# Kernel tuning notes

Measured on AMD Instinct MI355X. Metric: run time of the kernel, lower is better.

Reference implementation:

```python
import jax, jax.numpy as jnp
import numpy as np

N, DIN, D, HID, E, OUT = 16384, 1024, 1024, 256, 10, 1024


def setup_inputs() -> dict:
    key = jax.random.key(0)
    ks = jax.random.split(key, 13)
    g = lambda k, sh, s=0.02: (jax.random.normal(k, sh, jnp.float32) * s)
    return {
        "x": jax.random.normal(ks[0], (N, DIN), jnp.float32),
        "top_k": 2,
        # input projection (input_dim -> adjusted_dim)
        "Wp": g(ks[1], (DIN, D)), "bp": jnp.zeros((D,), jnp.float32),
        # MHA with seq_len=1 reduces exactly to out_proj(v_proj(x))
        "Wv": g(ks[2], (D, D)), "bv": jnp.zeros((D,), jnp.float32),
        "Wo": g(ks[3], (D, D)), "bo": jnp.zeros((D,), jnp.float32),
        # gate
        "Wg": g(ks[4], (D, E)), "bg": jnp.zeros((E,), jnp.float32),
        # experts: Linear(D,256) -> ReLU -> Linear(256,OUT), stacked over E
        "W1": g(ks[5], (E, D, HID)), "b1": jnp.zeros((E, HID), jnp.float32),
        "W2": g(ks[6], (E, HID, OUT)), "b2": jnp.zeros((E, OUT), jnp.float32),
    }


def reference(x, top_k, Wp, bp, Wv, bv, Wo, bo, Wg, bg, W1, b1, W2, b2):
    n = x.shape[0]
    e = Wg.shape[1]
    h = x @ Wp + bp                               # [N, D] input projection
    # MultiheadAttention with seq_len=1: softmax over one key == 1 exactly,
    # so attn output == out_proj(v_proj(h)).
    a = (h @ Wv + bv) @ Wo + bo                   # [N, D]
    gate_probs = jax.nn.softmax(a @ Wg + bg, axis=-1)   # [N, E]
    vals, idx = jax.lax.top_k(gate_probs, top_k)        # [N, K]
    vals = vals / jnp.sum(vals, axis=-1, keepdims=True)
    # scatter normalized top-k probs into dense combine weights [N, E]
    combine = jnp.zeros((n, e), a.dtype).at[jnp.arange(n)[:, None], idx].set(vals)
    # dense all-expert MLP, masked by combine weights (zeros kill unrouted experts)
    hid = jax.nn.relu(jnp.einsum("nd,edh->enh", a, W1) + b1[:, None, :])  # [E, N, HID]
    hid = hid * combine.T[:, :, None]                                      # weight tokens
    out = jnp.einsum("enh,eho->no", hid, W2) + combine @ b2                # [N, OUT]
    return out
```

## Files before the change

kernel.cpp:

```cpp
#include <hip/hip_runtime.h>
#include <hip/hip_bf16.h>
#include <math.h>

#define N_TOK   16384
#define D_IN    1024
#define D_MODEL 1024
#define HID     256
#define NEXP    10
#define D_OUT   1024

#define EPAD 128
#define A_CAP (2*N_TOK + NEXP*EPAD)

typedef __attribute__((ext_vector_type(8))) __bf16 bf16x8;
typedef __attribute__((ext_vector_type(4))) float floatx4;

__device__ __forceinline__ int xcd_chunk(int orig, int nwg)
{
    const int q = nwg >> 3, r = nwg & 7;
    const int c = orig & 7, j = orig >> 3;
    return (c < r ? c * (q + 1) : r * (q + 1) + (c - r) * q) + j;
}

__device__ __forceinline__ bf16x8 lds_frag(const short* base, int row, int chunk)
{
    return *(const bf16x8*)(base + row * 64 + (chunk << 3));
}

__device__ __forceinline__ void tile_plain(const short* As, const short* Bs,
                                           int wm, int wn, int lane, floatx4 acc[4][4])
{
    const int m15 = lane & 15, quad = lane >> 4, sw = m15 & 7;
#pragma unroll
    for (int kk = 0; kk < 2; ++kk) {
        bf16x8 af[4], bfr[4];
#pragma unroll
        for (int i = 0; i < 4; ++i)
            af[i] = lds_frag(As, wm * 64 + i * 16 + m15, ((kk << 2) + quad) ^ sw);
#pragma unroll
        for (int j = 0; j < 4; ++j)
            bfr[j] = lds_frag(Bs, wn * 64 + j * 16 + m15, ((kk << 2) + quad) ^ sw);
#pragma unroll
        for (int i = 0; i < 4; ++i)
#pragma unroll
            for (int j = 0; j < 4; ++j)
                acc[i][j] = __builtin_amdgcn_mfma_f32_16x16x32_bf16(af[i], bfr[j],
                                                                    acc[i][j], 0, 0, 0);
    }
}

__device__ __forceinline__ void tile_split(const short* As, const short* Bs,
                                           int wm, int wn, int lane, floatx4 acc[4][4])
{
    const int m15 = lane & 15, quad = lane >> 4, sw = m15 & 7;
    bf16x8 ah[4], al[4], bh[4], bl[4];
#pragma unroll
    for (int i = 0; i < 4; ++i) {
        int r = wm * 64 + i * 16 + m15;
        ah[i] = lds_frag(As, r, quad ^ sw);
        al[i] = lds_frag(As, r, (4 + quad) ^ sw);
    }
#pragma unroll
    for (int j = 0; j < 4; ++j) {
        int r = wn * 64 + j * 16 + m15;
        bh[j] = lds_frag(Bs, r, quad ^ sw);
        bl[j] = lds_frag(Bs, r, (4 + quad) ^ sw);
    }
#pragma unroll
    for (int i = 0; i < 4; ++i)
#pragma unroll
        for (int j = 0; j < 4; ++j) {
            floatx4 c = acc[i][j];
            c = __builtin_amdgcn_mfma_f32_16x16x32_bf16(ah[i], bh[j], c, 0, 0, 0);
            c = __builtin_amdgcn_mfma_f32_16x16x32_bf16(ah[i], bl[j], c, 0, 0, 0);
            c = __builtin_amdgcn_mfma_f32_16x16x32_bf16(al[i], bh[j], c, 0, 0, 0);
            acc[i][j] = c;
        }
}

__global__ __launch_bounds__(256)
void gemm_split_kernel(const __hip_bfloat16* Ahi_, const __hip_bfloat16* Alo_,
                       const __hip_bfloat16* Bhi_, const __hip_bfloat16* Blo_,
                       const float* __restrict__ bias,
                       __hip_bfloat16* Chi_, __hip_bfloat16* Clo_, int K, int N)
{
    __shared__ __align__(16) short As[128 * 64];
    __shared__ __align__(16) short Bs[128 * 64];
    const short* Ahi = (const short*)Ahi_;
    const short* Alo = (const short*)Alo_;
    const short* Bhi = (const short*)Bhi_;
    const short* Blo = (const short*)Blo_;

    const int tid = threadIdx.x, lane = tid & 63, w = tid >> 6;
    const int wm = w & 1, wn = w >> 1;
    const int lin = blockIdx.y * gridDim.x + blockIdx.x;
    const int lgc = xcd_chunk(lin, gridDim.x * gridDim.y);
    const int row0 = (lgc / gridDim.x) * 128, col0 = (lgc % gridDim.x) * 128;
    const int lr = lane >> 3;
    const int g = (lane & 7) ^ lr;
    const int plane = g >> 2, colel = (g & 3) * 8;

    const short* pA[4];
    const short* pB[4];
#pragma unroll
    for (int i = 0; i < 4; ++i) {
        int r = w * 32 + i * 8 + lr;
        pA[i] = (plane ? Alo : Ahi) + (size_t)(row0 + r) * K + colel;
        pB[i] = (plane ? Blo : Bhi) + (size_t)(col0 + r) * K + colel;
    }

    floatx4 acc[4][4];
#pragma unroll
    for (int i = 0; i < 4; ++i)
#pragma unroll
        for (int j = 0; j < 4; ++j) acc[i][j] = (floatx4)(0.f);

    bf16x8 va[4], vb[4];
#pragma unroll
    for (int i = 0; i < 4; ++i) {
        va[i] = *(const bf16x8*)(pA[i]);
        vb[i] = *(const bf16x8*)(pB[i]);
    }

    for (int k0 = 0; k0 < K; k0 += 32) {
        __syncthreads();
#pragma unroll
        for (int i = 0; i < 4; ++i) {
            *(bf16x8*)(&As[(w * 32 + i * 8) * 64 + lane * 8]) = va[i];
            *(bf16x8*)(&Bs[(w * 32 + i * 8) * 64 + lane * 8]) = vb[i];
        }
        __syncthreads();
        if (k0 + 32 < K) {
#pragma unroll
            for (int i = 0; i < 4; ++i) {
                va[i] = *(const bf16x8*)(pA[i] + k0 + 32);
                vb[i] = *(const bf16x8*)(pB[i] + k0 + 32);
            }
        }
        tile_split(As, Bs, wm, wn, lane, acc);
    }

    const int m15 = lane & 15, quad = lane >> 4;
#pragma unroll
    for (int i = 0; i < 4; ++i) {
#pragma unroll
        for (int t = 0; t < 4; ++t) {
            int row = row0 + wm * 64 + i * 16 + quad * 4 + t;
            size_t rb = (size_t)row * N;
#pragma unroll
            for (int j = 0; j < 4; ++j) {
                int col = col0 + wn * 64 + j * 16 + m15;
                float v = acc[i][j][t] + bias[col];
                __hip_bfloat16 hi = __float2bfloat16(v);
                Chi_[rb + col] = hi;
                if (Clo_) Clo_[rb + col] = __float2bfloat16(v - __bfloat162float(hi));
            }
        }
    }
}

__global__ __launch_bounds__(256)
void expert1_kernel(const __hip_bfloat16* a_, const __hip_bfloat16* W1t_,
                    const float* __restrict__ b1,
                    const int* __restrict__ assign_token, const int* __restrict__ offs,
                    const __hip_bfloat16* zrow_, __hip_bfloat16* hid_)
{
    __shared__ __align__(16) short As[128 * 64];
    __shared__ __align__(16) short Bs[128 * 64];
    const short* A = (const short*)a_;
    const short* zrow = (const short*)zrow_;

    const int tid = threadIdx.x, lane = tid & 63, w = tid >> 6;
    const int wm = w & 1, wn = w >> 1;
    const int lin = blockIdx.y * gridDim.x + blockIdx.x;
    const int lgc = xcd_chunk(lin, gridDim.x * gridDim.y);
    const int row0 = (lgc / gridDim.x) * 128, col0 = (lgc % gridDim.x) * 128;
    const int lr = lane >> 3, g = (lane & 7) ^ lr, colel = g * 8;

    int e = NEXP - 1;
    for (int q = 0; q < NEXP; ++q) { if (row0 < offs[q + 1]) { e = q; break; } }
    const short* B = (const short*)W1t_ + (size_t)e * HID * D_MODEL;

    const short* pA[4];
    const short* pB[4];
#pragma unroll
    for (int i = 0; i < 4; ++i) {
        int r = w * 32 + i * 8 + lr;
        int tok = assign_token[row0 + r];
        pA[i] = (tok >= 0 ? A + (size_t)tok * D_MODEL : zrow) + colel;
        pB[i] = B + (size_t)(col0 + r) * D_MODEL + colel;
    }

    floatx4 acc[4][4];
#pragma unroll
    for (int i = 0; i < 4; ++i)
#pragma unroll
        for (int j = 0; j < 4; ++j) acc[i][j] = (floatx4)(0.f);

    bf16x8 va[4], vb[4];
#pragma unroll
    for (int i = 0; i < 4; ++i) {
        va[i] = *(const bf16x8*)(pA[i]);
        vb[i] = *(const bf16x8*)(pB[i]);
    }

    for (int k0 = 0; k0 < D_MODEL; k0 += 64) {
        __syncthreads();
#pragma unroll
        for (int i = 0; i < 4; ++i) {
            *(bf16x8*)(&As[(w * 32 + i * 8) * 64 + lane * 8]) = va[i];
            *(bf16x8*)(&Bs[(w * 32 + i * 8) * 64 + lane * 8]) = vb[i];
        }
        __syncthreads();
        if (k0 + 64 < D_MODEL) {
#pragma unroll
            for (int i = 0; i < 4; ++i) {
                va[i] = *(const bf16x8*)(pA[i] + k0 + 64);
                vb[i] = *(const bf16x8*)(pB[i] + k0 + 64);
            }
        }
        tile_plain(As, Bs, wm, wn, lane, acc);
    }

    const int m15 = lane & 15, quad = lane >> 4;
#pragma unroll
    for (int i = 0; i < 4; ++i) {
#pragma unroll
        for (int t = 0; t < 4; ++t) {
            int row = row0 + wm * 64 + i * 16 + quad * 4 + t;
            size_t rb = (size_t)row * HID;
#pragma unroll
            for (int j = 0; j < 4; ++j) {
                int col = col0 + wn * 64 + j * 16 + m15;
                float v = acc[i][j][t] + b1[(size_t)e * HID + col];
                hid_[rb + col] = __float2bfloat16(fmaxf(v, 0.f));
            }
        }
    }
}

__global__ __launch_bounds__(256)
void expert2_kernel(const __hip_bfloat16* hid_, const __hip_bfloat16* W2t_,
                    const int* __restrict__ offs, __hip_bfloat16* exp_out_)
{
    __shared__ __align__(16) short As[128 * 64];
    __shared__ __align__(16) short Bs[128 * 64];
    const short* A = (const short*)hid_;

    const int tid = threadIdx.x, lane = tid & 63, w = tid >> 6;
    const int wm = w & 1, wn = w >> 1;
    const int lin = blockIdx.y * gridDim.x + blockIdx.x;
    const int lgc = xcd_chunk(lin, gridDim.x * gridDim.y);
    const int row0 = (lgc / gridDim.x) * 128, col0 = (lgc % gridDim.x) * 128;
    const int lr = lane >> 3, g = (lane & 7) ^ lr, colel = g * 8;

    int e = NEXP - 1;
    for (int q = 0; q < NEXP; ++q) { if (row0 < offs[q + 1]) { e = q; break; } }
    const short* B = (const short*)W2t_ + (size_t)e * D_OUT * HID;

    const short* pA[4];
    const short* pB[4];
#pragma unroll
    for (int i = 0; i < 4; ++i) {
        int r = w * 32 + i * 8 + lr;
        pA[i] = A + (size_t)(row0 + r) * HID + colel;
        pB[i] = B + (size_t)(col0 + r) * HID + colel;
    }

    floatx4 acc[4][4];
#pragma unroll
    for (int i = 0; i < 4; ++i)
#pragma unroll
        for (int j = 0; j < 4; ++j) acc[i][j] = (floatx4)(0.f);

    bf16x8 va[4], vb[4];
#pragma unroll
    for (int i = 0; i < 4; ++i) {
        va[i] = *(const bf16x8*)(pA[i]);
        vb[i] = *(const bf16x8*)(pB[i]);
    }

    for (int k0 = 0; k0 < HID; k0 += 64) {
        __syncthreads();
#pragma unroll
        for (int i = 0; i < 4; ++i) {
            *(bf16x8*)(&As[(w * 32 + i * 8) * 64 + lane * 8]) = va[i];
            *(bf16x8*)(&Bs[(w * 32 + i * 8) * 64 + lane * 8]) = vb[i];
        }
        __syncthreads();
        if (k0 + 64 < HID) {
#pragma unroll
            for (int i = 0; i < 4; ++i) {
                va[i] = *(const bf16x8*)(pA[i] + k0 + 64);
                vb[i] = *(const bf16x8*)(pB[i] + k0 + 64);
            }
        }
        tile_plain(As, Bs, wm, wn, lane, acc);
    }

    const int m15 = lane & 15, quad = lane >> 4;
#pragma unroll
    for (int i = 0; i < 4; ++i) {
#pragma unroll
        for (int t = 0; t < 4; ++t) {
            int row = row0 + wm * 64 + i * 16 + quad * 4 + t;
            size_t rb = (size_t)row * D_OUT;
#pragma unroll
            for (int j = 0; j < 4; ++j) {
                int col = col0 + wn * 64 + j * 16 + m15;
                exp_out_[rb + col] = __float2bfloat16(acc[i][j][t]);
            }
        }
    }
}

__global__ __launch_bounds__(256)
void convert_gate_kernel(const float* __restrict__ x, const float* __restrict__ MgT,
                         const float* __restrict__ bgeff,
                         __hip_bfloat16* __restrict__ x_hi, __hip_bfloat16* __restrict__ x_lo,
                         int* __restrict__ route_e, float* __restrict__ route_w)
{
    const int wave = threadIdx.x >> 6, lane = threadIdx.x & 63;
    const int n = blockIdx.x * 4 + wave;
    const float* xrow = x + (size_t)n * D_IN;

    float4 v[4];
#pragma unroll
    for (int it = 0; it < 4; ++it)
        v[it] = *(const float4*)(xrow + it * 256 + lane * 4);

    float p[NEXP];
#pragma unroll
    for (int e = 0; e < NEXP; ++e) p[e] = 0.f;

#pragma unroll
    for (int it = 0; it < 4; ++it) {
        const int d = it * 256 + lane * 4;
        union { __hip_bfloat16 b[4]; short4 s; } uh, ul;
        uh.b[0] = __float2bfloat16(v[it].x); ul.b[0] = __float2bfloat16(v[it].x - __bfloat162float(uh.b[0]));
        uh.b[1] = __float2bfloat16(v[it].y); ul.b[1] = __float2bfloat16(v[it].y - __bfloat162float(uh.b[1]));
        uh.b[2] = __float2bfloat16(v[it].z); ul.b[2] = __float2bfloat16(v[it].z - __bfloat162float(uh.b[2]));
        uh.b[3] = __float2bfloat16(v[it].w); ul.b[3] = __float2bfloat16(v[it].w - __bfloat162float(uh.b[3]));
        *(short4*)(x_hi + (size_t)n * D_IN + d) = uh.s;
        *(short4*)(x_lo + (size_t)n * D_IN + d) = ul.s;
#pragma unroll
        for (int e = 0; e < NEXP; ++e) {
            const float4 m = *(const float4*)(MgT + (size_t)e * 1024 + d);
            p[e] += v[it].x * m.x + v[it].y * m.y + v[it].z * m.z + v[it].w * m.w;
        }
    }

#pragma unroll
    for (int e = 0; e < NEXP; ++e) {
        float t = p[e];
        for (int off = 32; off > 0; off >>= 1) t += __shfl_down(t, off);
        p[e] = t;
    }
    if (lane == 0) {
        float lg[NEXP];
#pragma unroll
        for (int e = 0; e < NEXP; ++e) lg[e] = p[e] + bgeff[e];
        int e0 = 0; float v0 = lg[0];
        for (int e = 1; e < NEXP; ++e) if (lg[e] > v0) { v0 = lg[e]; e0 = e; }
        int e1 = -1; float v1 = -3.0e38f;
        for (int e = 0; e < NEXP; ++e) {
            if (e == e0) continue;
            if (lg[e] > v1) { v1 = lg[e]; e1 = e; }
        }
        float w0 = 1.f / (1.f + expf(v1 - v0));
        float w1 = 1.f - w0;
        route_e[n * 2]     = e0;
        route_e[n * 2 + 1] = e1;
        route_w[n * 2]     = w0;
        route_w[n * 2 + 1] = w1;
    }
}

__global__ __launch_bounds__(256)
void count_kernel(const int* __restrict__ route_e, int* __restrict__ counts)
{
    __shared__ int h[NEXP];
    if (threadIdx.x < NEXP) h[threadIdx.x] = 0;
    __syncthreads();
    const int i = blockIdx.x * 512 + threadIdx.x;
    atomicAdd(&h[route_e[i]], 1);
    atomicAdd(&h[route_e[i + 256]], 1);
    __syncthreads();
    if (threadIdx.x < NEXP) atomicAdd(&counts[threadIdx.x], h[threadIdx.x]);
}

__global__ __launch_bounds__(256)
void transpose_cvt_kernel(const float* __restrict__ in, __hip_bfloat16* out_hi,
                          __hip_bfloat16* out_lo, int R, int C)
{
    __shared__ float t[32][33];
    const size_t zoff = (size_t)blockIdx.z * R * C;
    in += zoff; out_hi += zoff; if (out_lo) out_lo += zoff;
    const int c0 = blockIdx.x * 32, r0 = blockIdx.y * 32;
    const int tx = threadIdx.x & 31, ty = threadIdx.x >> 5;
#pragma unroll
    for (int i = 0; i < 4; ++i)
        t[ty + i * 8][tx] = in[(size_t)(r0 + ty + i * 8) * C + (c0 + tx)];
    __syncthreads();
#pragma unroll
    for (int i = 0; i < 4; ++i) {
        float v = t[tx][ty + i * 8];
        size_t o = (size_t)(c0 + ty + i * 8) * R + (r0 + tx);
        __hip_bfloat16 hi = __float2bfloat16(v);
        out_hi[o] = hi;
        if (out_lo) out_lo[o] = __float2bfloat16(v - __bfloat162float(hi));
    }
}

__global__ __launch_bounds__(256)
void convert_plain_kernel(const float* __restrict__ in,
                          __hip_bfloat16* __restrict__ out_hi,
                          __hip_bfloat16* __restrict__ out_lo)
{
    const int i = blockIdx.x * 256 + threadIdx.x;
    const float4 v = ((const float4*)in)[i];
    union { __hip_bfloat16 b[4]; short4 s; } uh, ul;
    uh.b[0] = __float2bfloat16(v.x); ul.b[0] = __float2bfloat16(v.x - __bfloat162float(uh.b[0]));
    uh.b[1] = __float2bfloat16(v.y); ul.b[1] = __float2bfloat16(v.y - __bfloat162float(uh.b[1]));
    uh.b[2] = __float2bfloat16(v.z); ul.b[2] = __float2bfloat16(v.z - __bfloat162float(uh.b[2]));
    uh.b[3] = __float2bfloat16(v.w); ul.b[3] = __float2bfloat16(v.w - __bfloat162float(uh.b[3]));
    ((short4*)out_hi)[i] = uh.s;
    ((short4*)out_lo)[i] = ul.s;
}

__global__ __launch_bounds__(256)
void bias2_kernel(const float* __restrict__ bp, const float* __restrict__ bv,
                  const float* __restrict__ bo,
                  const __hip_bfloat16* __restrict__ Pt_hi,
                  const __hip_bfloat16* __restrict__ Pt_lo,
                  const __hip_bfloat16* __restrict__ Wot_hi,
                  const __hip_bfloat16* __restrict__ Wot_lo,
                  float* __restrict__ beff2)
{
    const int wave = threadIdx.x >> 6, lane = threadIdx.x & 63;
    const int n = blockIdx.x * 4 + wave;
    float acc = 0.f;
    for (int k = lane; k < D_MODEL; k += 64) {
        const size_t o = (size_t)n * D_MODEL + k;
        float pt = __bfloat162float(Pt_hi[o]) + __bfloat162float(Pt_lo[o]);
        float wo = __bfloat162float(Wot_hi[o]) + __bfloat162float(Wot_lo[o]);
        acc += bp[k] * pt + bv[k] * wo;
    }
    for (int off = 32; off > 0; off >>= 1) acc += __shfl_down(acc, off);
    if (lane == 0) beff2[n] = acc + bo[n];
}

__global__ __launch_bounds__(256)
void wchain_kernel(const float* __restrict__ A, const float* __restrict__ B,
                   float* __restrict__ Cm, int trans)
{
    const int wave = threadIdx.x >> 6, lane = threadIdx.x & 63;
    const int m = blockIdx.x * 4 + wave;
    float acc[NEXP];
#pragma unroll
    for (int e = 0; e < NEXP; ++e) acc[e] = 0.f;
    const float* ar = A + (size_t)m * 1024;
    for (int d = lane; d < 1024; d += 64) {
        float av = ar[d];
        const float* br = B + (size_t)d * NEXP;
#pragma unroll
        for (int e = 0; e < NEXP; ++e) acc[e] += av * br[e];
    }
#pragma unroll
    for (int e = 0; e < NEXP; ++e) {
        float v = acc[e];
        for (int off = 32; off > 0; off >>= 1) v += __shfl_down(v, off);
        if (lane == 0) Cm[trans ? ((size_t)e * 1024 + m) : ((size_t)m * NEXP + e)] = v;
    }
}

__global__ __launch_bounds__(256)
void bias_eff_kernel(const float* __restrict__ bp, const float* __restrict__ bv,
                     const float* __restrict__ bo, const float* __restrict__ bg,
                     const float* __restrict__ Wg, const float* __restrict__ t1,
                     const float* __restrict__ t2, float* __restrict__ bgeff)
{
    __shared__ float red[256];
    const int tid = threadIdx.x;
    float acc[NEXP];
#pragma unroll
    for (int e = 0; e < NEXP; ++e) acc[e] = 0.f;
    for (int d = tid; d < 1024; d += 256) {
        float o = bo[d], v = bv[d], p = bp[d];
#pragma unroll
        for (int e = 0; e < NEXP; ++e)
            acc[e] += o * Wg[d * NEXP + e] + v * t1[d * NEXP + e] + p * t2[d * NEXP + e];
    }
    for (int e = 0; e < NEXP; ++e) {
        red[tid] = acc[e];
        __syncthreads();
        for (int s = 128; s > 0; s >>= 1) {
            if (tid < s) red[tid] += red[tid + s];
            __syncthreads();
        }
        if (tid == 0) bgeff[e] = red[0] + bg[e];
        __syncthreads();
    }
}

__global__ __launch_bounds__(256)
void init_kernel(int* __restrict__ counts, int* __restrict__ cursors,
                 int* __restrict__ assign_token, int* __restrict__ zrow_i,
                 float* __restrict__ fzero)
{
    int i = blockIdx.x * 256 + threadIdx.x;
    if (i < NEXP) { counts[i] = 0; cursors[i] = 0; }
    if (i < 512) zrow_i[i] = 0;
    if (i < 1024) fzero[i] = 0.f;
    if (i < A_CAP) assign_token[i] = -1;
}

__global__ void offsets_kernel(const int* __restrict__ counts, int* __restrict__ offs)
{
    if (threadIdx.x == 0 && blockIdx.x == 0) {
        int acc = 0;
        for (int e = 0; e < NEXP; ++e) {
            offs[e] = acc;
            acc += (counts[e] + EPAD - 1) / EPAD * EPAD;
        }
        offs[NEXP] = acc;
    }
}

__global__ __launch_bounds__(256)
void scatter_kernel(const int* __restrict__ route_e,
                    const int* __restrict__ offs, int* __restrict__ cursors,
                    int* __restrict__ assign_token, int* __restrict__ slot_of)
{
    const int i = blockIdx.x * 256 + threadIdx.x;
    const int lane = threadIdx.x & 63;
    const int e = route_e[i];
    int slot = 0;
#pragma unroll
    for (int q = 0; q < NEXP; ++q) {
        unsigned long long mask = __ballot(e == q);
        if (e == q) {
            const int leader = (int)__ffsll((long long)mask) - 1;
            const int rank = (int)__popcll(mask & ((1ull << lane) - 1ull));
            int base = 0;
            if (lane == leader) base = atomicAdd(&cursors[q], (int)__popcll(mask));
            base = __shfl(base, leader);
            slot = offs[q] + base + rank;
        }
    }
    assign_token[slot] = i >> 1;
    slot_of[i] = slot;
}

__global__ __launch_bounds__(256)
void combine_kernel(const __hip_bfloat16* __restrict__ exp_out,
                    const int* __restrict__ slot_of, const int* __restrict__ route_e,
                    const float* __restrict__ route_w, const float* __restrict__ b2,
                    float* __restrict__ out)
{
    const int n = blockIdx.x;
    const int c = threadIdx.x * 4;
    const int s0 = slot_of[n * 2],  s1 = slot_of[n * 2 + 1];
    const int e0 = route_e[n * 2],  e1 = route_e[n * 2 + 1];
    const float w0 = route_w[n * 2], w1 = route_w[n * 2 + 1];

    union U { float2 f2; __hip_bfloat16 b[4]; } u0, u1;
    u0.f2 = *(const float2*)(exp_out + (size_t)s0 * D_OUT + c);
    u1.f2 = *(const float2*)(exp_out + (size_t)s1 * D_OUT + c);
    const float4 bb0 = *(const float4*)(b2 + (size_t)e0 * D_OUT + c);
    const float4 bb1 = *(const float4*)(b2 + (size_t)e1 * D_OUT + c);

    float4 o;
    o.x = w0 * (__bfloat162float(u0.b[0]) + bb0.x) + w1 * (__bfloat162float(u1.b[0]) + bb1.x);
    o.y = w0 * (__bfloat162float(u0.b[1]) + bb0.y) + w1 * (__bfloat162float(u1.b[1]) + bb1.y);
    o.z = w0 * (__bfloat162float(u0.b[2]) + bb0.z) + w1 * (__bfloat162float(u1.b[2]) + bb1.z);
    o.w = w0 * (__bfloat162float(u0.b[3]) + bb0.w) + w1 * (__bfloat162float(u1.b[3]) + bb1.w);
    *(float4*)(out + (size_t)n * D_OUT + c) = o;
}

extern "C" void kernel_launch(void* const* d_in, const int* in_sizes, int n_in,
                              void* d_out, int out_size, void* d_ws, size_t ws_size,
                              hipStream_t stream)
{
    const float* x  = (const float*)d_in[0];
    const float* Wp = (const float*)d_in[2];
    const float* bp = (const float*)d_in[3];
    const float* Wv = (const float*)d_in[4];
    const float* bv = (const float*)d_in[5];
    const float* Wo = (const float*)d_in[6];
    const float* bo = (const float*)d_in[7];
    const float* Wg = (const float*)d_in[8];
    const float* bg = (const float*)d_in[9];
    const float* W1 = (const float*)d_in[10];
    const float* b1 = (const float*)d_in[11];
    const float* W2 = (const float*)d_in[12];
    const float* b2 = (const float*)d_in[13];
    float* out = (float*)d_out;

    char* W = (char*)d_ws;
    typedef __hip_bfloat16 bf;
    bf* x_hi  = (bf*)(W + 0);
    bf* x_lo  = (bf*)(W + 33554432);
    bf* a_bf  = (bf*)(W + 100663296);
    bf* exp_out = (bf*)(W + 0);
    bf* hid   = (bf*)(W + 69730304);
    bf* Wvr_hi = (bf*)(W + 88080384);
    bf* Wvr_lo = (bf*)(W + 90177536);
    bf* Wpr_hi = (bf*)(W + 92274688);
    bf* Wpr_lo = (bf*)(W + 94371840);
    float* fzero = (float*)(W + 96468992);
    float* beff2 = (float*)(W + 96473088);
    bf* Pt_hi  = (bf*)(W + 134217728);
    bf* Pt_lo  = (bf*)(W + 136314880);
    bf* Mt_hi  = (bf*)(W + 138412032);
    bf* Mt_lo  = (bf*)(W + 140509184);
    bf* Wot_hi = (bf*)(W + 142606336);
    bf* Wot_lo = (bf*)(W + 144703488);
    bf* W1t    = (bf*)(W + 146800640);
    bf* W2t    = (bf*)(W + 152043520);
    bf*    zrow         = (bf*)(W + 157286400);
    int*   route_e      = (int*)(W + 157288448);
    float* route_w      = (float*)(W + 157419520);
    int*   slot_of      = (int*)(W + 157550592);
    int*   assign_token = (int*)(W + 157681664);
    int*   counts       = (int*)(W + 157817856);
    int*   offs         = (int*)(W + 157817920);
    int*   cursors      = (int*)(W + 157817984);
    float* MgT          = (float*)(W + 157818048);
    float* t1           = (float*)(W + 157859008);
    float* t2           = (float*)(W + 157899968);
    float* bgeff        = (float*)(W + 157940928);

    dim3 blk(256);

    init_kernel<<<(A_CAP + 255) / 256, blk, 0, stream>>>(counts, cursors, assign_token,
                                                         (int*)zrow, fzero);

    transpose_cvt_kernel<<<dim3(32, 32, 1), blk, 0, stream>>>(Wo, Wot_hi, Wot_lo, D_MODEL, D_MODEL);
    convert_plain_kernel<<<1024, blk, 0, stream>>>(Wv, Wvr_hi, Wvr_lo);
    convert_plain_kernel<<<1024, blk, 0, stream>>>(Wp, Wpr_hi, Wpr_lo);
    transpose_cvt_kernel<<<dim3(HID / 32, D_MODEL / 32, NEXP), blk, 0, stream>>>(W1, W1t, nullptr, D_MODEL, HID);
    transpose_cvt_kernel<<<dim3(D_OUT / 32, HID / 32, NEXP), blk, 0, stream>>>(W2, W2t, nullptr, HID, D_OUT);

    wchain_kernel<<<256, blk, 0, stream>>>(Wo, Wg, t1, 0);
    wchain_kernel<<<256, blk, 0, stream>>>(Wv, t1, t2, 0);
    wchain_kernel<<<256, blk, 0, stream>>>(Wp, t2, MgT, 1);
    bias_eff_kernel<<<1, blk, 0, stream>>>(bp, bv, bo, bg, Wg, t1, t2, bgeff);

    dim3 pgrid(D_MODEL / 128, D_MODEL / 128);
    gemm_split_kernel<<<pgrid, blk, 0, stream>>>(Wot_hi, Wot_lo, Wvr_hi, Wvr_lo, fzero,
                                                 Pt_hi, Pt_lo, D_MODEL, D_MODEL);
    gemm_split_kernel<<<pgrid, blk, 0, stream>>>(Pt_hi, Pt_lo, Wpr_hi, Wpr_lo, fzero,
                                                 Mt_hi, Mt_lo, D_MODEL, D_IN);
    bias2_kernel<<<D_MODEL / 4, blk, 0, stream>>>(bp, bv, bo, Pt_hi, Pt_lo,
                                                  Wot_hi, Wot_lo, beff2);

    convert_gate_kernel<<<N_TOK / 4, blk, 0, stream>>>(x, MgT, bgeff, x_hi, x_lo,
                                                       route_e, route_w);
    count_kernel<<<2 * N_TOK / 512, blk, 0, stream>>>(route_e, counts);
    offsets_kernel<<<1, 64, 0, stream>>>(counts, offs);
    scatter_kernel<<<2 * N_TOK / 256, blk, 0, stream>>>(route_e, offs, cursors,
                                                        assign_token, slot_of);

    dim3 cgrid(D_MODEL / 128, N_TOK / 128);
    gemm_split_kernel<<<cgrid, blk, 0, stream>>>(x_hi, x_lo, Mt_hi, Mt_lo, beff2,
                                                 a_bf, nullptr, D_IN, D_MODEL);

    expert1_kernel<<<dim3(HID / 128, A_CAP / 128), blk, 0, stream>>>(
        a_bf, W1t, b1, assign_token, offs, zrow, hid);
    expert2_kernel<<<dim3(D_OUT / 128, A_CAP / 128), blk, 0, stream>>>(
        hid, W2t, offs, exp_out);
    combine_kernel<<<N_TOK, blk, 0, stream>>>(exp_out, slot_of, route_e, route_w, b2, out);
}
```

Baseline: 558.0 us.

## Fold dense projection chain into per-expert W1 weights, skip activation GEMM

```diff
diff --git a/kernel.cpp b/kernel.cpp
--- a/kernel.cpp
+++ b/kernel.cpp
@@ -82,7 +82,8 @@
 void gemm_split_kernel(const __hip_bfloat16* Ahi_, const __hip_bfloat16* Alo_,
                        const __hip_bfloat16* Bhi_, const __hip_bfloat16* Blo_,
                        const float* __restrict__ bias,
-                       __hip_bfloat16* Chi_, __hip_bfloat16* Clo_, int K, int N)
+                       __hip_bfloat16* Chi_, __hip_bfloat16* Clo_, int K, int N,
+                       size_t zsA, size_t zsB, size_t zsC)
 {
     __shared__ __align__(16) short As[128 * 64];
     __shared__ __align__(16) short Bs[128 * 64];
@@ -90,6 +91,90 @@
     const short* Alo = (const short*)Alo_;
     const short* Bhi = (const short*)Bhi_;
     const short* Blo = (const short*)Blo_;
+
+    const int tid = threadIdx.x, lane = tid & 63, w = tid >> 6;
+    const int wm = w & 1, wn = w >> 1;
+    const size_t zA = (size_t)blockIdx.z * zsA;
+    const size_t zB = (size_t)blockIdx.z * zsB;
+    const size_t zC = (size_t)blockIdx.z * zsC;
+    const int lin = blockIdx.y * gridDim.x + blockIdx.x;
+    const int lgc = xcd_chunk(lin, gridDim.x * gridDim.y);
+    const int row0 = (lgc / gridDim.x) * 128, col0 = (lgc % gridDim.x) * 128;
+    const int lr = lane >> 3;
+    const int g = (lane & 7) ^ lr;
+    const int plane = g >> 2, colel = (g & 3) * 8;
+
+    const short* pA[4];
+    const short* pB[4];
+#pragma unroll
+    for (int i = 0; i < 4; ++i) {
+        int r = w * 32 + i * 8 + lr;
+        pA[i] = (plane ? Alo : Ahi) + zA + (size_t)(row0 + r) * K + colel;
+        pB[i] = (plane ? Blo : Bhi) + zB + (size_t)(col0 + r) * K + colel;
+    }
+
+    floatx4 acc[4][4];
+#pragma unroll
+    for (int i = 0; i < 4; ++i)
+#pragma unroll
+        for (int j = 0; j < 4; ++j) acc[i][j] = (floatx4)(0.f);
+
+    bf16x8 va[4], vb[4];
+#pragma unroll
+    for (int i = 0; i < 4; ++i) {
+        va[i] = *(const bf16x8*)(pA[i]);
+        vb[i] = *(const bf16x8*)(pB[i]);
+    }
+
+    for (int k0 = 0; k0 < K; k0 += 32) {
+        __syncthreads();
+#pragma unroll
+        for (int i = 0; i < 4; ++i) {
+            *(bf16x8*)(&As[(w * 32 + i * 8) * 64 + lane * 8]) = va[i];
+            *(bf16x8*)(&Bs[(w * 32 + i * 8) * 64 + lane * 8]) = vb[i];
+        }
+        __syncthreads();
+        if (k0 + 32 < K) {
+#pragma unroll
+            for (int i = 0; i < 4; ++i) {
+                va[i] = *(const bf16x8*)(pA[i] + k0 + 32);
+                vb[i] = *(const bf16x8*)(pB[i] + k0 + 32);
+            }
+        }
+        tile_split(As, Bs, wm, wn, lane, acc);
+    }
+
+    const int m15 = lane & 15, quad = lane >> 4;
+#pragma unroll
+    for (int i = 0; i < 4; ++i) {
+#pragma unroll
+        for (int t = 0; t < 4; ++t) {
+            int row = row0 + wm * 64 + i * 16 + quad * 4 + t;
+            size_t rb = zC + (size_t)row * N;
+#pragma unroll
+            for (int j = 0; j < 4; ++j) {
+                int col = col0 + wn * 64 + j * 16 + m15;
+                float v = acc[i][j][t] + bias[col];
+                __hip_bfloat16 hi = __float2bfloat16(v);
+                Chi_[rb + col] = hi;
+                if (Clo_) Clo_[rb + col] = __float2bfloat16(v - __bfloat162float(hi));
+            }
+        }
+    }
+}
+
+__global__ __launch_bounds__(256)
+void expert1_kernel(const __hip_bfloat16* x_hi_, const __hip_bfloat16* x_lo_,
+                    const __hip_bfloat16* W1e_hi_, const __hip_bfloat16* W1e_lo_,
+                    const float* __restrict__ b1eff,
+                    const int* __restrict__ assign_token, const int* __restrict__ offs,
+                    const __hip_bfloat16* zrow_, __hip_bfloat16* hid_)
+{
+    __shared__ __align__(16) short As[128 * 64];
+    __shared__ __align__(16) short Bs[128 * 64];
+    const short* Xhi = (const short*)x_hi_;
+    const short* Xlo = (const short*)x_lo_;
+    const short* zrow = (const short*)zrow_;
 
     const int tid = threadIdx.x, lane = tid & 63, w = tid >> 6;
     const int wm = w & 1, wn = w >> 1;
@@ -100,13 +185,19 @@
     const int g = (lane & 7) ^ lr;
     const int plane = g >> 2, colel = (g & 3) * 8;
 
+    int e = NEXP - 1;
+    for (int q = 0; q < NEXP; ++q) { if (row0 < offs[q + 1]) { e = q; break; } }
+    const short* Bh = (const short*)W1e_hi_ + (size_t)e * HID * D_IN;
+    const short* Bl = (const short*)W1e_lo_ + (size_t)e * HID * D_IN;
+
     const short* pA[4];
     const short* pB[4];
 #pragma unroll
     for (int i = 0; i < 4; ++i) {
         int r = w * 32 + i * 8 + lr;
-        pA[i] = (plane ? Alo : Ahi) + (size_t)(row0 + r) * K + colel;
-        pB[i] = (plane ? Blo : Bhi) + (size_t)(col0 + r) * K + colel;
+        int tok = assign_token[row0 + r];
+        pA[i] = (tok >= 0 ? (plane ? Xlo : Xhi) + (size_t)tok * D_IN : zrow) + colel;
+        pB[i] = (plane ? Bl : Bh) + (size_t)(col0 + r) * D_IN + colel;
     }
 
     floatx4 acc[4][4];
@@ -122,7 +213,7 @@
         vb[i] = *(const bf16x8*)(pB[i]);
     }
 
-    for (int k0 = 0; k0 < K; k0 += 32) {
+    for (int k0 = 0; k0 < D_IN; k0 += 32) {
         __syncthreads();
 #pragma unroll
         for (int i = 0; i < 4; ++i) {
@@ -130,7 +221,7 @@
             *(bf16x8*)(&Bs[(w * 32 + i * 8) * 64 + lane * 8]) = vb[i];
         }
         __syncthreads();
-        if (k0 + 32 < K) {
+        if (k0 + 32 < D_IN) {
 #pragma unroll
             for (int i = 0; i < 4; ++i) {
                 va[i] = *(const bf16x8*)(pA[i] + k0 + 32);
@@ -146,93 +237,11 @@
 #pragma unroll
         for (int t = 0; t < 4; ++t) {
             int row = row0 + wm * 64 + i * 16 + quad * 4 + t;
-            size_t rb = (size_t)row * N;
+            size_t rb = (size_t)row * HID;
 #pragma unroll
             for (int j = 0; j < 4; ++j) {
                 int col = col0 + wn * 64 + j * 16 + m15;
-                float v = acc[i][j][t] + bias[col];
-                __hip_bfloat16 hi = __float2bfloat16(v);
-                Chi_[rb + col] = hi;
-                if (Clo_) Clo_[rb + col] = __float2bfloat16(v - __bfloat162float(hi));
-            }
-        }
-    }
-}
-
-__global__ __launch_bounds__(256)
-void expert1_kernel(const __hip_bfloat16* a_, const __hip_bfloat16* W1t_,
-                    const float* __restrict__ b1,
-                    const int* __restrict__ assign_token, const int* __restrict__ offs,
-                    const __hip_bfloat16* zrow_, __hip_bfloat16* hid_)
-{
-    __shared__ __align__(16) short As[128 * 64];
-    __shared__ __align__(16) short Bs[128 * 64];
-    const short* A = (const short*)a_;
-    const short* zrow = (const short*)zrow_;
-
-    const int tid = threadIdx.x, lane = tid & 63, w = tid >> 6;
-    const int wm = w & 1, wn = w >> 1;
-    const int lin = blockIdx.y * gridDim.x + blockIdx.x;
-    const int lgc = xcd_chunk(lin, gridDim.x * gridDim.y);
-    const int row0 = (lgc / gridDim.x) * 128, col0 = (lgc % gridDim.x) * 128;
-    const int lr = lane >> 3, g = (lane & 7) ^ lr, colel = g * 8;
-
-    int e = NEXP - 1;
-    for (int q = 0; q < NEXP; ++q) { if (row0 < offs[q + 1]) { e = q; break; } }
-    const short* B = (const short*)W1t_ + (size_t)e * HID * D_MODEL;
-
-    const short* pA[4];
-    const short* pB[4];
-#pragma unroll
-    for (int i = 0; i < 4; ++i) {
-        int r = w * 32 + i * 8 + lr;
-        int tok = assign_token[row0 + r];
-        pA[i] = (tok >= 0 ? A + (size_t)tok * D_MODEL : zrow) + colel;
-        pB[i] = B + (size_t)(col0 + r) * D_MODEL + colel;
-    }
-
-    floatx4 acc[4][4];
-#pragma unroll
-    for (int i = 0; i < 4; ++i)
-#pragma unroll
-        for (int j = 0; j < 4; ++j) acc[i][j] = (floatx4)(0.f);
-
-    bf16x8 va[4], vb[4];
-#pragma unroll
-    for (int i = 0; i < 4; ++i) {
-        va[i] = *(const bf16x8*)(pA[i]);
-        vb[i] = *(const bf16x8*)(pB[i]);
-    }
-
-    for (int k0 = 0; k0 < D_MODEL; k0 += 64) {
-        __syncthreads();
-#pragma unroll
-        for (int i = 0; i < 4; ++i) {
-            *(bf16x8*)(&As[(w * 32 + i * 8) * 64 + lane * 8]) = va[i];
-            *(bf16x8*)(&Bs[(w * 32 + i * 8) * 64 + lane * 8]) = vb[i];
-        }
-        __syncthreads();
-        if (k0 + 64 < D_MODEL) {
-#pragma unroll
-            for (int i = 0; i < 4; ++i) {
-                va[i] = *(const bf16x8*)(pA[i] + k0 + 64);
-                vb[i] = *(const bf16x8*)(pB[i] + k0 + 64);
-            }
-        }
-        tile_plain(As, Bs, wm, wn, lane, acc);
-    }
-
-    const int m15 = lane & 15, quad = lane >> 4;
-#pragma unroll
-    for (int i = 0; i < 4; ++i) {
-#pragma unroll
-        for (int t = 0; t < 4; ++t) {
-            int row = row0 + wm * 64 + i * 16 + quad * 4 + t;
-            size_t rb = (size_t)row * HID;
-#pragma unroll
-            for (int j = 0; j < 4; ++j) {
-                int col = col0 + wn * 64 + j * 16 + m15;
-                float v = acc[i][j][t] + b1[(size_t)e * HID + col];
+                float v = acc[i][j][t] + b1eff[(size_t)e * HID + col];
                 hid_[rb + col] = __float2bfloat16(fmaxf(v, 0.f));
             }
         }
@@ -448,6 +457,23 @@
     }
     for (int off = 32; off > 0; off >>= 1) acc += __shfl_down(acc, off);
     if (lane == 0) beff2[n] = acc + bo[n];
+}
+
+__global__ __launch_bounds__(256)
+void b1eff_kernel(const float* __restrict__ beff2,
+                  const __hip_bfloat16* __restrict__ W1t_hi,
+                  const __hip_bfloat16* __restrict__ W1t_lo,
+                  const float* __restrict__ b1, float* __restrict__ b1eff)
+{
+    const int wave = threadIdx.x >> 6, lane = threadIdx.x & 63;
+    const int n = blockIdx.x * 4 + wave;
+    const size_t base = (size_t)n * D_MODEL;
+    float acc = 0.f;
+    for (int k = lane; k < D_MODEL; k += 64)
+        acc += beff2[k] * (__bfloat162float(W1t_hi[base + k]) +
+                           __bfloat162float(W1t_lo[base + k]));
+    for (int off = 32; off > 0; off >>= 1) acc += __shfl_down(acc, off);
+    if (lane == 0) b1eff[n] = acc + b1[n];
 }
 
 __global__ __launch_bounds__(256)
@@ -601,7 +627,6 @@
     typedef __hip_bfloat16 bf;
     bf* x_hi  = (bf*)(W + 0);
     bf* x_lo  = (bf*)(W + 33554432);
-    bf* a_bf  = (bf*)(W + 100663296);
     bf* exp_out = (bf*)(W + 0);
     bf* hid   = (bf*)(W + 69730304);
     bf* Wvr_hi = (bf*)(W + 88080384);
@@ -610,10 +635,14 @@
     bf* Wpr_lo = (bf*)(W + 94371840);
     float* fzero = (float*)(W + 96468992);
     float* beff2 = (float*)(W + 96473088);
+    bf* W1t_lo   = (bf*)(W + 100663296);
+    bf* W1eff_hi = (bf*)(W + 105906176);
+    bf* W1eff_lo = (bf*)(W + 111149056);
+    float* b1eff = (float*)(W + 116391936);
     bf* Pt_hi  = (bf*)(W + 134217728);
     bf* Pt_lo  = (bf*)(W + 136314880);
-    bf* Mt_hi  = (bf*)(W + 138412032);
-    bf* Mt_lo  = (bf*)(W + 140509184);
+    bf* Mrow_hi = (bf*)(W + 138412032);
+    bf* Mrow_lo = (bf*)(W + 140509184);
     bf* Wot_hi = (bf*)(W + 142606336);
     bf* Wot_lo = (bf*)(W + 144703488);
     bf* W1t    = (bf*)(W + 146800640);
@@ -639,7 +668,7 @@
     transpose_cvt_kernel<<<dim3(32, 32, 1), blk, 0, stream>>>(Wo, Wot_hi, Wot_lo, D_MODEL, D_MODEL);
     convert_plain_kernel<<<1024, blk, 0, stream>>>(Wv, Wvr_hi, Wvr_lo);
     convert_plain_kernel<<<1024, blk, 0, stream>>>(Wp, Wpr_hi, Wpr_lo);
-    transpose_cvt_kernel<<<dim3(HID / 32, D_MODEL / 32, NEXP), blk, 0, stream>>>(W1, W1t, nullptr, D_MODEL, HID);
+    transpose_cvt_kernel<<<dim3(HID / 32, D_MODEL / 32, NEXP), blk, 0, stream>>>(W1, W1t, W1t_lo, D_MODEL, HID);
     transpose_cvt_kernel<<<dim3(D_OUT / 32, HID / 32, NEXP), blk, 0, stream>>>(W2, W2t, nullptr, HID, D_OUT);
 
     wchain_kernel<<<256, blk, 0, stream>>>(Wo, Wg, t1, 0);
@@ -647,13 +676,19 @@
     wchain_kernel<<<256, blk, 0, stream>>>(Wp, t2, MgT, 1);
     bias_eff_kernel<<<1, blk, 0, stream>>>(bp, bv, bo, bg, Wg, t1, t2, bgeff);
 
-    dim3 pgrid(D_MODEL / 128, D_MODEL / 128);
+    dim3 pgrid(D_MODEL / 128, D_MODEL / 128, 1);
     gemm_split_kernel<<<pgrid, blk, 0, stream>>>(Wot_hi, Wot_lo, Wvr_hi, Wvr_lo, fzero,
-                                                 Pt_hi, Pt_lo, D_MODEL, D_MODEL);
-    gemm_split_kernel<<<pgrid, blk, 0, stream>>>(Pt_hi, Pt_lo, Wpr_hi, Wpr_lo, fzero,
-                                                 Mt_hi, Mt_lo, D_MODEL, D_IN);
+                                                 Pt_hi, Pt_lo, D_MODEL, D_MODEL, 0, 0, 0);
+    gemm_split_kernel<<<pgrid, blk, 0, stream>>>(Wpr_hi, Wpr_lo, Pt_hi, Pt_lo, fzero,
+                                                 Mrow_hi, Mrow_lo, D_MODEL, D_MODEL, 0, 0, 0);
     bias2_kernel<<<D_MODEL / 4, blk, 0, stream>>>(bp, bv, bo, Pt_hi, Pt_lo,
                                                   Wot_hi, Wot_lo, beff2);
+    b1eff_kernel<<<NEXP * HID / 4, blk, 0, stream>>>(beff2, W1t, W1t_lo, b1, b1eff);
+    dim3 wgrid(D_IN / 128, HID / 128, NEXP);
+    gemm_split_kernel<<<wgrid, blk, 0, stream>>>(W1t, W1t_lo, Mrow_hi, Mrow_lo, fzero,
+                                                 W1eff_hi, W1eff_lo, D_MODEL, D_IN,
+                                                 (size_t)HID * D_MODEL, 0,
+                                                 (size_t)HID * D_IN);
 
     convert_gate_kernel<<<N_TOK / 4, blk, 0, stream>>>(x, MgT, bgeff, x_hi, x_lo,
                                                        route_e, route_w);
@@ -662,12 +697,8 @@
     scatter_kernel<<<2 * N_TOK / 256, blk, 0, stream>>>(route_e, offs, cursors,
                                                         assign_token, slot_of);
 
-    dim3 cgrid(D_MODEL / 128, N_TOK / 128);
-    gemm_split_kernel<<<cgrid, blk, 0, stream>>>(x_hi, x_lo, Mt_hi, Mt_lo, beff2,
-                                                 a_bf, nullptr, D_IN, D_MODEL);
-
     expert1_kernel<<<dim3(HID / 128, A_CAP / 128), blk, 0, stream>>>(
-        a_bf, W1t, b1, assign_token, offs, zrow, hid);
+        x_hi, x_lo, W1eff_hi, W1eff_lo, b1eff, assign_token, offs, zrow, hid);
     expert2_kernel<<<dim3(D_OUT / 128, A_CAP / 128), blk, 0, stream>>>(
         hid, W2t, offs, exp_out);
     combine_kernel<<<N_TOK, blk, 0, stream>>>(exp_out, slot_of, route_e, route_w, b2, out);
```

Result: faster. 536.0 us (-3.9%).
